# Performance work log

Hardware: AMD Instinct MI355X
Metric: run time of the kernel (lower is better)

The kernel has to match this reference:

```python
import jax, jax.numpy as jnp
import numpy as np

SPATIAL = 128   # N: wall spatial resolution
CROP = 256      # M: temporal bins (power of 2)
BIN_LEN = 0.01
WALL_SIZE = 2.0


def _grids():
    # Reproduces parpareparam(): normalized freq-domain coordinate grids, [2M,2N,2N].
    M, N = CROP, SPATIAL
    width = WALL_SIZE / 2.0
    trange = CROP * BIN_LEN  # crop * c * (bin_len / c)
    zdim = (np.arange(2 * M, dtype=np.float32) - M) / M
    xdim = (np.arange(2 * N, dtype=np.float32) - N) / N
    gz = np.ascontiguousarray(np.broadcast_to(zdim[:, None, None], (2 * M, 2 * N, 2 * N)))
    gy = np.ascontiguousarray(np.broadcast_to(xdim[None, :, None], (2 * M, 2 * N, 2 * N)))
    gx = np.ascontiguousarray(np.broadcast_to(xdim[None, None, :], (2 * M, 2 * N, 2 * N)))
    fkrange = (N * trange / (M * width * 4.0)) ** 2
    gznew = np.sqrt(fkrange * (gx ** 2 + gy ** 2) + gz ** 2).astype(np.float32)
    return jnp.asarray(gx), jnp.asarray(gy), jnp.asarray(gz), jnp.asarray(gznew)


def _grid_sample_3d(vol, x, y, z):
    """Trilinear grid sample, padding_mode='zeros', align_corners=False.
    vol: [B, D, H, W] (complex ok); x/y/z: [Dg,Hg,Wg] in [-1,1] (x->W, y->H, z->D)."""
    B, D, H, W = vol.shape
    ix = ((x + 1.0) * W - 1.0) * 0.5
    iy = ((y + 1.0) * H - 1.0) * 0.5
    iz = ((z + 1.0) * D - 1.0) * 0.5
    ix0 = jnp.floor(ix); iy0 = jnp.floor(iy); iz0 = jnp.floor(iz)
    fx = ix - ix0; fy = iy - iy0; fz = iz - iz0
    ix0 = ix0.astype(jnp.int32); iy0 = iy0.astype(jnp.int32); iz0 = iz0.astype(jnp.int32)
    out = jnp.zeros((B,) + x.shape, vol.dtype)
    for dz in (0, 1):
        for dy in (0, 1):
            for dx in (0, 1):
                xi = ix0 + dx; yi = iy0 + dy; zi = iz0 + dz
                valid = (xi >= 0) & (xi < W) & (yi >= 0) & (yi < H) & (zi >= 0) & (zi < D)
                w = ((fx if dx else 1.0 - fx) * (fy if dy else 1.0 - fy) * (fz if dz else 1.0 - fz))
                w = jnp.where(valid, w, 0.0)
                xi = jnp.clip(xi, 0, W - 1); yi = jnp.clip(yi, 0, H - 1); zi = jnp.clip(zi, 0, D - 1)
                out = out + vol[:, zi, yi, xi] * w  # gather 8 trilinear corners
    return out


def _fk_forward(feat_padded):
    # feat_padded: [B, Dn, CROP, N, N] float32
    B, Dn, T, H, W = feat_padded.shape
    M, N = CROP, SPATIAL
    gx, gy, gz, gznew = _grids()
    gridz = jnp.arange(M, dtype=jnp.float32) / (M - 1)  # gridz_1xMx1x1
    data = feat_padded.reshape(B * Dn, M, N, N) * (gridz ** 2)[None, :, None, None]
    data = jax.nn.relu(data)
    # sqrt with grad-safe double-where (torch sqrt backward at 0 is nan; math limit here is 0)
    data = jnp.where(data > 0, jnp.sqrt(jnp.where(data > 0, data, 1.0)), 0.0)
    pad = jnp.zeros((B * Dn, 2 * M, 2 * N, 2 * N), jnp.float32).at[:, :M, :N, :N].set(data)
    fre = jnp.fft.fftn(pad, axes=(1, 2, 3))            # torch.rfft(x,3,onesided=False)
    fre = jnp.roll(fre, (M, N, N), axis=(1, 2, 3))      # fftshift rolls
    t = _grid_sample_3d(fre, gx, gy, gznew)             # Stolt frequency resampling
    t = t.at[:, :M + 1].set(0.0)                        # z0pos = M+1 (first zdim>0)
    t = t * (jnp.abs(gz) / (gznew + 1e-8))[None]        # |f_z| Jacobian scaling
    t = jnp.roll(t, (M, N, N), axis=(1, 2, 3))          # ifftshift (even dims)
    vol = jnp.fft.ifftn(t, axes=(1, 2, 3))[:, :M, :N, :N]
    out = vol.real ** 2 + vol.imag ** 2                 # squared magnitude
    return out.reshape(B, Dn, M, N, N)


def setup_inputs() -> dict:
    key = jax.random.key(0)
    feat = jax.random.uniform(key, (1, 1, CROP, SPATIAL, SPATIAL), dtype=jnp.float32)
    return {"feture_bxdxtxhxw": feat, "tbes": 0, "tens": CROP}


def reference(feture_bxdxtxhxw, tbes, tens):
    tbe, ten = int(tbes), int(tens)
    featpad = jnp.pad(feture_bxdxtxhxw, ((0, 0), (0, 0), (tbe, CROP - ten), (0, 0), (0, 0)))
    return _fk_forward(featpad)
```

## Files before the change

### kernel.cpp

```cpp
#include <hip/hip_runtime.h>


typedef float __attribute__((ext_vector_type(2))) cpx;

__device__ float4 g_tw4[512];

__device__ __forceinline__ cpx cswap(cpx a){ return __builtin_shufflevector(a, a, 1, 0); }
__device__ __forceinline__ cpx cmji(cpx a){ return cswap(a)*(cpx){1.0f, -1.0f}; }
__device__ __forceinline__ cpx cmpi(cpx a){ return cswap(a)*(cpx){-1.0f, 1.0f}; }

__device__ __forceinline__ int rev4_8(int k){
    return ((k & 3) << 6) | ((k & 12) << 2) | ((k >> 2) & 12) | (k >> 6);
}
__device__ __forceinline__ int rev8_9(int k){
    return ((k & 7) << 6) | (k & 56) | (k >> 6);
}

__global__ void k_tw(){
    int j = threadIdx.x;
    double a = -2.0*3.14159265358979323846*(double)j/512.0;
    float c = (float)cos(a), s = (float)sin(a);
    g_tw4[j] = make_float4(c, c, -s, s);
}

template<bool INV>
__device__ __forceinline__ cpx twmul(cpx a, int k){
    float4 t = g_tw4[k & 511];
    cpx wl = {t.x, t.y};
    cpx wh = {t.z, t.w};
    cpx r = a*wl;
    return INV ? (r - cswap(a)*wh) : (r + cswap(a)*wh);
}

template<bool INV>
__device__ __forceinline__ void dft4(cpx* x){
    cpx e0 = x[0] + x[2], e1 = x[0] - x[2];
    cpx o0 = x[1] + x[3], o1 = x[1] - x[3];
    x[0] = e0 + o0;
    x[2] = e0 - o0;
    cpx j1 = INV ? cmpi(o1) : cmji(o1);
    x[1] = e1 + j1;
    x[3] = e1 - j1;
}

template<bool INV>
__device__ __forceinline__ void dft4_h2(cpx* x){
    cpx a0 = x[0], a1 = x[1];
    x[0] = a0 + a1;
    x[2] = a0 - a1;
    cpx j1 = INV ? cmpi(a1) : cmji(a1);
    x[1] = a0 + j1;
    x[3] = a0 - j1;
}

template<bool INV>
__device__ __forceinline__ void dft4_lo2(cpx* x){
    cpx e0 = x[0] + x[2], e1 = x[0] - x[2];
    cpx o0 = x[1] + x[3], o1 = x[1] - x[3];
    x[0] = e0 + o0;
    x[1] = e1 + (INV ? cmpi(o1) : cmji(o1));
}

template<bool INV>
__device__ __forceinline__ void dft8(cpx* x){
    const float s = 0.70710678118654752440f;
    cpx e0 = x[0] + x[4], e2 = x[0] - x[4];
    cpx e1 = x[2] + x[6], e3 = x[2] - x[6];
    cpx E0 = e0 + e1, E2 = e0 - e1;
    cpx j3 = INV ? cmpi(e3) : cmji(e3);
    cpx E1 = e2 + j3, E3 = e2 - j3;
    cpx o0 = x[1] + x[5], o2 = x[1] - x[5];
    cpx o1 = x[3] + x[7], o3 = x[3] - x[7];
    cpx O0 = o0 + o1, O2 = o0 - o1;
    cpx k3 = INV ? cmpi(o3) : cmji(o3);
    cpx O1 = o2 + k3, O3 = o2 - k3;
    cpx W1, W2, W3;
    if (!INV){
        W1 = s*(O1 + cmji(O1));
        W2 = cmji(O2);
        W3 = s*(cmji(O3) - O3);
    } else {
        W1 = s*(O1 + cmpi(O1));
        W2 = cmpi(O2);
        W3 = s*(cmpi(O3) - O3);
    }
    x[0] = E0 + O0; x[4] = E0 - O0;
    x[1] = E1 + W1; x[5] = E1 - W1;
    x[2] = E2 + W2; x[6] = E2 - W2;
    x[3] = E3 + W3; x[7] = E3 - W3;
}

template<bool INV>
__device__ __forceinline__ void dft8_h4(cpx* x){
    const float s = 0.70710678118654752440f;
    cpx a0 = x[0], a1 = x[1], a2 = x[2], a3 = x[3];
    cpx E0 = a0 + a2, E2 = a0 - a2;
    cpx j3 = INV ? cmpi(a2) : cmji(a2);
    cpx E1 = a0 + j3, E3 = a0 - j3;
    cpx O0 = a1 + a3, O2 = a1 - a3;
    cpx k3 = INV ? cmpi(a3) : cmji(a3);
    cpx O1 = a1 + k3, O3 = a1 - k3;
    cpx W1, W2, W3;
    if (!INV){
        W1 = s*(O1 + cmji(O1));
        W2 = cmji(O2);
        W3 = s*(cmji(O3) - O3);
    } else {
        W1 = s*(O1 + cmpi(O1));
        W2 = cmpi(O2);
        W3 = s*(cmpi(O3) - O3);
    }
    x[0] = E0 + O0; x[4] = E0 - O0;
    x[1] = E1 + W1; x[5] = E1 - W1;
    x[2] = E2 + W2; x[6] = E2 - W2;
    x[3] = E3 + W3; x[7] = E3 - W3;
}

template<bool INV>
__device__ __forceinline__ void dft8_lo4(cpx* x){
    const float s = 0.70710678118654752440f;
    cpx e0 = x[0] + x[4], e2 = x[0] - x[4];
    cpx e1 = x[2] + x[6], e3 = x[2] - x[6];
    cpx E0 = e0 + e1, E2 = e0 - e1;
    cpx j3 = INV ? cmpi(e3) : cmji(e3);
    cpx E1 = e2 + j3, E3 = e2 - j3;
    cpx o0 = x[1] + x[5], o2 = x[1] - x[5];
    cpx o1 = x[3] + x[7], o3 = x[3] - x[7];
    cpx O0 = o0 + o1, O2 = o0 - o1;
    cpx k3 = INV ? cmpi(o3) : cmji(o3);
    cpx O1 = o2 + k3, O3 = o2 - k3;
    cpx W1, W2, W3;
    if (!INV){
        W1 = s*(O1 + cmji(O1));
        W2 = cmji(O2);
        W3 = s*(cmji(O3) - O3);
    } else {
        W1 = s*(O1 + cmpi(O1));
        W2 = cmpi(O2);
        W3 = s*(cmpi(O3) - O3);
    }
    x[0] = E0 + O0;
    x[1] = E1 + W1;
    x[2] = E2 + W2;
    x[3] = E3 + W3;
}

template<bool INV, bool CROP>
__device__ __forceinline__ void fft256_r4_tail(cpx* sl, int b){
    cpx x[4];
    {
        int j = b & 15, g = (b >> 4) << 6;
        #pragma unroll
        for (int t = 0; t < 4; ++t) x[t] = sl[g + j + (t << 4)];
        dft4<INV>(x);
        #pragma unroll
        for (int r = 1; r < 4; ++r) x[r] = twmul<INV>(x[r], 8*j*r);
        #pragma unroll
        for (int r = 0; r < 4; ++r) sl[g + j + (r << 4)] = x[r];
    }
    __syncthreads();
    {
        int j = b & 3, g = (b >> 2) << 4;
        #pragma unroll
        for (int t = 0; t < 4; ++t) x[t] = sl[g + j + (t << 2)];
        dft4<INV>(x);
        #pragma unroll
        for (int r = 1; r < 4; ++r) x[r] = twmul<INV>(x[r], 32*j*r);
        #pragma unroll
        for (int r = 0; r < 4; ++r) sl[g + j + (r << 2)] = x[r];
    }
    __syncthreads();
    {
        int g = b << 2;
        #pragma unroll
        for (int t = 0; t < 4; ++t) x[t] = sl[g + t];
        if (CROP){
            dft4_lo2<INV>(x);
            sl[g] = x[0]; sl[g + 1] = x[1];
        } else {
            dft4<INV>(x);
            #pragma unroll
            for (int r = 0; r < 4; ++r) sl[g + r] = x[r];
        }
    }
    __syncthreads();
}

__global__ __launch_bounds__(256) void k_fft_x_fill(const float* __restrict__ feat, cpx* __restrict__ V){
    __shared__ cpx s[4*256];
    int tid = threadIdx.x;
    int line0 = blockIdx.x << 2;
    int l = tid >> 6, b = tid & 63;
    int line = line0 + l;
    cpx* sl = s + l*256;
    {
        int z = line >> 7;
        float g = (float)z*(1.0f/255.0f);
        const float* fl = feat + ((size_t)line << 7);
        float a  = fl[b]*g*g;       a  = a  > 0.0f ? sqrtf(a)  : 0.0f;
        float bb = fl[b + 64]*g*g;  bb = bb > 0.0f ? sqrtf(bb) : 0.0f;
        cpx x[4];
        x[0] = (cpx){a, 0.0f};
        x[1] = (cpx){bb, 0.0f};
        dft4_h2<false>(x);
        #pragma unroll
        for (int r = 1; r < 4; ++r) x[r] = twmul<false>(x[r], 2*b*r);
        #pragma unroll
        for (int r = 0; r < 4; ++r) sl[b + (r << 6)] = x[r];
    }
    __syncthreads();
    fft256_r4_tail<false, false>(sl, b);
    for (int i = tid; i < 4*128; i += 256){
        int ll = i >> 7, f4 = i & 127;
        int lin = line0 + ll;
        int base = ((lin >> 7) << 16) + ((lin & 127) << 8);
        const cpx* sll = s + ll*256;
        int e0 = 2*f4;
        cpx Fm = e0 ? sll[rev4_8(e0 - 1) ^ 2] : (cpx){0.0f, 0.0f};
        cpx F0 = sll[rev4_8(e0) ^ 2];
        cpx F1 = sll[rev4_8(e0 + 1) ^ 2];
        cpx o0 = 0.5f*(Fm + F0);
        cpx o1 = 0.5f*(F0 + F1);
        float4 o = make_float4(o0.x, o0.y, o1.x, o1.y);
        ((float4*)(V + base))[f4] = o;
    }
}

__global__ __launch_bounds__(256) void k_fft_x_inv_mag(const cpx* __restrict__ W,
                                                       float* __restrict__ out){
    __shared__ cpx s[4*256];
    int tid = threadIdx.x;
    int line0 = blockIdx.x << 2;
    int l = tid >> 6, b = tid & 63;
    int line = line0 + l;
    int base = ((line >> 7) << 16) + ((line & 127) << 8);
    cpx* sl = s + l*256;
    {
        cpx x[4];
        #pragma unroll
        for (int t = 0; t < 4; ++t) x[t] = W[base + b + (t << 6)];
        dft4<true>(x);
        #pragma unroll
        for (int r = 1; r < 4; ++r) x[r] = twmul<true>(x[r], 2*b*r);
        #pragma unroll
        for (int r = 0; r < 4; ++r) sl[b + (r << 6)] = x[r];
    }
    __syncthreads();
    fft256_r4_tail<true, true>(sl, b);
    {
        int z = line >> 7, y = line & 127;
        cpx v0 = sl[rev4_8(2*b)];
        cpx v1 = sl[rev4_8(2*b + 1)];
        const float SC2 = (1.0f/33554432.0f)*(1.0f/33554432.0f);
        float2 o = make_float2((v0.x*v0.x + v0.y*v0.y)*SC2,
                               (v1.x*v1.x + v1.y*v1.y)*SC2);
        ((float2*)(out + (((size_t)(z*128 + y)) << 7)))[b] = o;
    }
}

template<bool INV, bool HALF_IN, bool HALF_OUT>
__global__ __launch_bounds__(1024) void k_fft_y(cpx* __restrict__ V){
    __shared__ cpx s[256*16];
    int tid = threadIdx.x;
    int z  = blockIdx.x >> 4;
    int x0 = (blockIdx.x & 15) << 4;
    int base = (z << 16) + x0;
    int c = tid & 15, idx = tid >> 4;
    cpx x[4];
    {
        int j = idx;
        if (HALF_IN){
            x[0] = V[base + (j << 8) + c];
            x[1] = V[base + ((j + 64) << 8) + c];
            dft4_h2<INV>(x);
        } else {
            #pragma unroll
            for (int t = 0; t < 4; ++t) x[t] = V[base + ((j + (t << 6)) << 8) + c];
            dft4<INV>(x);
        }
        #pragma unroll
        for (int r = 1; r < 4; ++r) x[r] = twmul<INV>(x[r], 2*j*r);
        #pragma unroll
        for (int r = 0; r < 4; ++r) s[(j + (r << 6))*16 + c] = x[r];
    }
    __syncthreads();
    {
        int j = idx & 15, g = (idx >> 4) << 6;
        #pragma unroll
        for (int t = 0; t < 4; ++t) x[t] = s[(g + j + (t << 4))*16 + c];
        dft4<INV>(x);
        #pragma unroll
        for (int r = 1; r < 4; ++r) x[r] = twmul<INV>(x[r], 8*j*r);
        #pragma unroll
        for (int r = 0; r < 4; ++r) s[(g + j + (r << 4))*16 + c] = x[r];
    }
    __syncthreads();
    {
        int j = idx & 3, g = (idx >> 2) << 4;
        #pragma unroll
        for (int t = 0; t < 4; ++t) x[t] = s[(g + j + (t << 2))*16 + c];
        dft4<INV>(x);
        #pragma unroll
        for (int r = 1; r < 4; ++r) x[r] = twmul<INV>(x[r], 32*j*r);
        #pragma unroll
        for (int r = 0; r < 4; ++r) s[(g + j + (r << 2))*16 + c] = x[r];
    }
    __syncthreads();
    if (HALF_OUT){
        int g = idx << 2;
        #pragma unroll
        for (int t = 0; t < 4; ++t) x[t] = s[(g + t)*16 + c];
        dft4_lo2<INV>(x);
        int e0 = rev4_8(g);
        V[base + (e0 << 8) + c] = x[0];
        V[base + ((e0 + 64) << 8) + c] = x[1];
        return;
    }
    {
        int g = idx << 2;
        #pragma unroll
        for (int t = 0; t < 4; ++t) x[t] = s[(g + t)*16 + c];
        dft4<INV>(x);
        #pragma unroll
        for (int r = 0; r < 4; ++r) s[(g + r)*16 + c] = x[r];
    }
    __syncthreads();
    for (int i = tid; i < 256*8; i += 1024){
        int f4c = i & 7, e = i >> 3;
        int p0 = rev4_8(e) ^ 2;
        float4 S0 = ((const float4*)(s + p0*16))[f4c];
        float4 S1 = make_float4(0.0f, 0.0f, 0.0f, 0.0f);
        if (e){
            int p1 = rev4_8(e - 1) ^ 2;
            S1 = ((const float4*)(s + p1*16))[f4c];
        }
        float4 o;
        o.x = 0.5f*(S0.x + S1.x); o.y = 0.5f*(S0.y + S1.y);
        o.z = 0.5f*(S0.z + S1.z); o.w = 0.5f*(S0.w + S1.w);
        ((float4*)(V + base + (e << 8)))[f4c] = o;
    }
}

__global__ __launch_bounds__(1024, 8) void k_fftz_fused(cpx* __restrict__ V){
    __shared__ cpx s[512*16];
    int tid = threadIdx.x;
    int yD  = blockIdx.x >> 4;
    int x0D = (blockIdx.x & 15) << 4;
    int baseD = (yD << 8) + x0D;
    int yS  = (yD + 128) & 255;
    int x0S = (x0D + 128) & 255;
    int baseS = (yS << 8) + x0S;
    int c = tid & 15, idx = tid >> 4;
    cpx x[8];
    int j = idx;
    {
        #pragma unroll
        for (int t = 0; t < 4; ++t)
            x[t] = V[baseS + (((size_t)(j + (t << 6))) << 16) + c];
        dft8_h4<false>(x);
        #pragma unroll
        for (int r = 1; r < 8; ++r) x[r] = twmul<false>(x[r], j*r);
        #pragma unroll
        for (int r = 0; r < 8; ++r) s[(j + (r << 6))*16 + c] = x[r];
    }
    __syncthreads();
    {
        int jj = idx & 7, g = (idx >> 3) << 6;
        #pragma unroll
        for (int t = 0; t < 8; ++t) x[t] = s[(g + jj + (t << 3))*16 + c];
        dft8<false>(x);
        #pragma unroll
        for (int r = 1; r < 8; ++r) x[r] = twmul<false>(x[r], 8*jj*r);
        #pragma unroll
        for (int r = 0; r < 8; ++r) s[(g + jj + (r << 3))*16 + c] = x[r];
    }
    __syncthreads();
    {
        int g = idx << 3;
        #pragma unroll
        for (int t = 0; t < 8; ++t) x[t] = s[(g + t)*16 + c];
        dft8_lo4<false>(x);
        #pragma unroll
        for (int r = 0; r < 4; ++r){
            int e = (r << 6) | ((idx & 7) << 3) | (idx >> 3);
            s[e*16 + c] = x[r];
        }
    }
    __syncthreads();
    {
        int xs = x0S + c;
        float gx = (float)(xs - 128)*(1.0f/128.0f);
        float gy = (float)(yS - 128)*(1.0f/128.0f);
        float rxy = 0.1024f*(gx*gx + gy*gy);
        #pragma unroll
        for (int t = 0; t < 4; ++t){
            int zd = j + (t << 6);
            cpx r = (cpx){0.0f, 0.0f};
            if (zd){
                float gz = (float)zd*(1.0f/256.0f);
                float gzn = sqrtf(rxy + gz*gz);
                float iz = ((gzn + 1.0f)*512.0f - 1.0f)*0.5f;
                float fiz = floorf(iz);
                int iz0 = (int)fiz;
                float fz = iz - fiz;
                float sc = gz/(gzn + 1e-8f);
                int b0 = (iz0 < 511 ? iz0 : 511) - 256;
                int b1 = ((iz0 + 1) < 511 ? (iz0 + 1) : 511) - 256;
                float w0 = (iz0     <= 511) ? (1.0f - fz)*sc : 0.0f;
                float w1 = (iz0 + 1 <= 511) ? fz*sc : 0.0f;
                cpx a = s[(b0 << 4) + c];
                cpx b = s[(b1 << 4) + c];
                r = a*w0 + b*w1;
            }
            x[t] = r;
        }
        dft8_h4<true>(x);
        #pragma unroll
        for (int r = 1; r < 8; ++r) x[r] = twmul<true>(x[r], j*r);
    }
    __syncthreads();
    {
        #pragma unroll
        for (int r = 0; r < 8; ++r) s[(j + (r << 6))*16 + c] = x[r];
    }
    __syncthreads();
    {
        int jj = idx & 7, g = (idx >> 3) << 6;
        #pragma unroll
        for (int t = 0; t < 8; ++t) x[t] = s[(g + jj + (t << 3))*16 + c];
        dft8<true>(x);
        #pragma unroll
        for (int r = 1; r < 8; ++r) x[r] = twmul<true>(x[r], 8*jj*r);
        #pragma unroll
        for (int r = 0; r < 8; ++r) s[(g + jj + (r << 3))*16 + c] = x[r];
    }
    __syncthreads();
    {
        int g = idx << 3;
        #pragma unroll
        for (int t = 0; t < 8; ++t) x[t] = s[(g + t)*16 + c];
        dft8_lo4<true>(x);
        #pragma unroll
        for (int r = 0; r < 4; ++r){
            int e = (r << 6) | ((idx & 7) << 3) | (idx >> 3);
            V[baseD + (((size_t)(e + 256)) << 16) + c] = x[r];
        }
    }
}

extern "C" void kernel_launch(void* const* d_in, const int* in_sizes, int n_in,
                              void* d_out, int out_size, void* d_ws, size_t ws_size,
                              hipStream_t stream){
    const float* feat = (const float*)d_in[0];
    float* out = (float*)d_out;

    const size_t WS_NEED = (size_t)512*256*256*8;
    if (ws_size < WS_NEED){
        hipMemsetAsync(d_out, 0, (size_t)out_size*sizeof(float), stream);
        return;
    }
    cpx* V  = (cpx*)d_ws;
    cpx* Vu = V + (size_t)256*65536;

    k_tw<<<1, 512, 0, stream>>>();
    k_fft_x_fill<<<8192, 256, 0, stream>>>(feat, V);
    k_fft_y<false, true, false><<<4096, 1024, 0, stream>>>(V);
    k_fftz_fused<<<4096, 1024, 0, stream>>>(V);
    k_fft_y<true, false, true><<<4096, 1024, 0, stream>>>(Vu);
    k_fft_x_inv_mag<<<8192, 256, 0, stream>>>(Vu, out);
}
```

Before: 258.6 us.

## Restructure Y-axis FFT as two radix-16 passes with 256-thread blocks

The 256-point Y-axis FFT goes from four radix-4 passes with 1024 threads per block to two in-register radix-16 passes (16x16 decomposition) with 256 threads per block. This removes two shared-memory round trips and barriers and pads the shared row stride to 18 to reduce bank conflicts. In exchange each thread holds 16 complex values, which raises register pressure and may lower occupancy. The launch configuration changes to match.

Measured after the change: 250.8 us. 3.0% less time.

```diff
diff --git a/kernel.cpp b/kernel.cpp
--- a/kernel.cpp
+++ b/kernel.cpp
@@ -2,6 +2,7 @@
 
 
 typedef float __attribute__((ext_vector_type(2))) cpx;
+typedef float __attribute__((ext_vector_type(4))) cpx2;
 
 __device__ float4 g_tw4[512];
 
@@ -12,9 +13,7 @@
 __device__ __forceinline__ int rev4_8(int k){
     return ((k & 3) << 6) | ((k & 12) << 2) | ((k >> 2) & 12) | (k >> 6);
 }
-__device__ __forceinline__ int rev8_9(int k){
-    return ((k & 7) << 6) | (k & 56) | (k >> 6);
-}
+__device__ __forceinline__ int prm(int q){ return ((q & 3) << 2) | (q >> 2); }
 
 __global__ void k_tw(){
     int j = threadIdx.x;
@@ -42,7 +41,6 @@
     x[1] = e1 + j1;
     x[3] = e1 - j1;
 }
-
 template<bool INV>
 __device__ __forceinline__ void dft4_h2(cpx* x){
     cpx a0 = x[0], a1 = x[1];
@@ -52,13 +50,59 @@
     x[1] = a0 + j1;
     x[3] = a0 - j1;
 }
-
 template<bool INV>
 __device__ __forceinline__ void dft4_lo2(cpx* x){
     cpx e0 = x[0] + x[2], e1 = x[0] - x[2];
     cpx o0 = x[1] + x[3], o1 = x[1] - x[3];
     x[0] = e0 + o0;
     x[1] = e1 + (INV ? cmpi(o1) : cmji(o1));
+}
+
+template<bool INV>
+__device__ __forceinline__ void dft16(cpx* x){
+    #pragma unroll
+    for (int j2 = 0; j2 < 4; ++j2){
+        cpx y[4] = {x[j2], x[j2+4], x[j2+8], x[j2+12]};
+        dft4<INV>(y);
+        if (j2){
+            #pragma unroll
+            for (int r = 1; r < 4; ++r) y[r] = twmul<INV>(y[r], 32*j2*r);
+        }
+        x[j2] = y[0]; x[j2+4] = y[1]; x[j2+8] = y[2]; x[j2+12] = y[3];
+    }
+    #pragma unroll
+    for (int g = 0; g < 16; g += 4) dft4<INV>(x + g);
+}
+template<bool INV>
+__device__ __forceinline__ void dft16_h8(cpx* x){
+    #pragma unroll
+    for (int j2 = 0; j2 < 4; ++j2){
+        cpx y[4];
+        y[0] = x[j2]; y[1] = x[j2+4];
+        dft4_h2<INV>(y);
+        if (j2){
+            #pragma unroll
+            for (int r = 1; r < 4; ++r) y[r] = twmul<INV>(y[r], 32*j2*r);
+        }
+        x[j2] = y[0]; x[j2+4] = y[1]; x[j2+8] = y[2]; x[j2+12] = y[3];
+    }
+    #pragma unroll
+    for (int g = 0; g < 16; g += 4) dft4<INV>(x + g);
+}
+template<bool INV>
+__device__ __forceinline__ void dft16_lo8(cpx* x){
+    #pragma unroll
+    for (int j2 = 0; j2 < 4; ++j2){
+        cpx y[4] = {x[j2], x[j2+4], x[j2+8], x[j2+12]};
+        dft4<INV>(y);
+        if (j2){
+            #pragma unroll
+            for (int r = 1; r < 4; ++r) y[r] = twmul<INV>(y[r], 32*j2*r);
+        }
+        x[j2] = y[0]; x[j2+4] = y[1]; x[j2+8] = y[2]; x[j2+12] = y[3];
+    }
+    #pragma unroll
+    for (int g = 0; g < 16; g += 4) dft4_lo2<INV>(x + g);
 }
 
 template<bool INV>
@@ -89,7 +133,6 @@
     x[2] = E2 + W2; x[6] = E2 - W2;
     x[3] = E3 + W3; x[7] = E3 - W3;
 }
-
 template<bool INV>
 __device__ __forceinline__ void dft8_h4(cpx* x){
     const float s = 0.70710678118654752440f;
@@ -115,7 +158,6 @@
     x[2] = E2 + W2; x[6] = E2 - W2;
     x[3] = E3 + W3; x[7] = E3 - W3;
 }
-
 template<bool INV>
 __device__ __forceinline__ void dft8_lo4(cpx* x){
     const float s = 0.70710678118654752440f;
@@ -258,86 +300,63 @@
     }
 }
 
+#define YROW 18
 template<bool INV, bool HALF_IN, bool HALF_OUT>
-__global__ __launch_bounds__(1024) void k_fft_y(cpx* __restrict__ V){
-    __shared__ cpx s[256*16];
+__global__ __launch_bounds__(256, 4) void k_fft_y(cpx* __restrict__ V){
+    __shared__ cpx s[256*YROW];
     int tid = threadIdx.x;
     int z  = blockIdx.x >> 4;
     int x0 = (blockIdx.x & 15) << 4;
     int base = (z << 16) + x0;
-    int c = tid & 15, idx = tid >> 4;
-    cpx x[4];
-    {
-        int j = idx;
+    int c = tid & 15, j = tid >> 4;
+    cpx x[16];
+    {
         if (HALF_IN){
-            x[0] = V[base + (j << 8) + c];
-            x[1] = V[base + ((j + 64) << 8) + c];
-            dft4_h2<INV>(x);
+            #pragma unroll
+            for (int t = 0; t < 8; ++t) x[t] = V[base + ((j + (t << 4)) << 8) + c];
+            dft16_h8<INV>(x);
         } else {
             #pragma unroll
-            for (int t = 0; t < 4; ++t) x[t] = V[base + ((j + (t << 6)) << 8) + c];
-            dft4<INV>(x);
-        }
-        #pragma unroll
-        for (int r = 1; r < 4; ++r) x[r] = twmul<INV>(x[r], 2*j*r);
-        #pragma unroll
-        for (int r = 0; r < 4; ++r) s[(j + (r << 6))*16 + c] = x[r];
-    }
-    __syncthreads();
-    {
-        int j = idx & 15, g = (idx >> 4) << 6;
-        #pragma unroll
-        for (int t = 0; t < 4; ++t) x[t] = s[(g + j + (t << 4))*16 + c];
-        dft4<INV>(x);
-        #pragma unroll
-        for (int r = 1; r < 4; ++r) x[r] = twmul<INV>(x[r], 8*j*r);
-        #pragma unroll
-        for (int r = 0; r < 4; ++r) s[(g + j + (r << 4))*16 + c] = x[r];
-    }
-    __syncthreads();
-    {
-        int j = idx & 3, g = (idx >> 2) << 4;
-        #pragma unroll
-        for (int t = 0; t < 4; ++t) x[t] = s[(g + j + (t << 2))*16 + c];
-        dft4<INV>(x);
-        #pragma unroll
-        for (int r = 1; r < 4; ++r) x[r] = twmul<INV>(x[r], 32*j*r);
-        #pragma unroll
-        for (int r = 0; r < 4; ++r) s[(g + j + (r << 2))*16 + c] = x[r];
-    }
-    __syncthreads();
+            for (int t = 0; t < 16; ++t) x[t] = V[base + ((j + (t << 4)) << 8) + c];
+            dft16<INV>(x);
+        }
+        #pragma unroll
+        for (int r = 1; r < 16; ++r) x[prm(r)] = twmul<INV>(x[prm(r)], 2*j*r);
+        #pragma unroll
+        for (int r = 0; r < 16; ++r) s[(j + (r << 4))*YROW + c] = x[prm(r)];
+    }
+    __syncthreads();
+    int g = j << 4;
     if (HALF_OUT){
-        int g = idx << 2;
-        #pragma unroll
-        for (int t = 0; t < 4; ++t) x[t] = s[(g + t)*16 + c];
-        dft4_lo2<INV>(x);
-        int e0 = rev4_8(g);
-        V[base + (e0 << 8) + c] = x[0];
-        V[base + ((e0 + 64) << 8) + c] = x[1];
+        #pragma unroll
+        for (int t = 0; t < 16; ++t) x[t] = s[(g + t)*YROW + c];
+        dft16_lo8<INV>(x);
+        #pragma unroll
+        for (int sb = 0; sb < 8; ++sb)
+            V[base + (((sb << 4) | j) << 8) + c] = x[prm(sb)];
         return;
     }
     {
-        int g = idx << 2;
-        #pragma unroll
-        for (int t = 0; t < 4; ++t) x[t] = s[(g + t)*16 + c];
-        dft4<INV>(x);
-        #pragma unroll
-        for (int r = 0; r < 4; ++r) s[(g + r)*16 + c] = x[r];
-    }
-    __syncthreads();
-    for (int i = tid; i < 256*8; i += 1024){
+        #pragma unroll
+        for (int t = 0; t < 16; ++t) x[t] = s[(g + t)*YROW + c];
+        dft16<INV>(x);
+        #pragma unroll
+        for (int u = 0; u < 16; ++u) s[(g + u)*YROW + c] = x[u];
+    }
+    __syncthreads();
+    for (int i = tid; i < 256*8; i += 256){
         int f4c = i & 7, e = i >> 3;
-        int p0 = rev4_8(e) ^ 2;
-        float4 S0 = ((const float4*)(s + p0*16))[f4c];
-        float4 S1 = make_float4(0.0f, 0.0f, 0.0f, 0.0f);
+        int k0 = e ^ 128;
+        int r0 = ((k0 & 15) << 4) | prm(k0 >> 4);
+        cpx2 S0 = ((const cpx2*)(s + r0*YROW))[f4c];
+        cpx2 S1 = (cpx2){0.0f, 0.0f, 0.0f, 0.0f};
         if (e){
-            int p1 = rev4_8(e - 1) ^ 2;
-            S1 = ((const float4*)(s + p1*16))[f4c];
-        }
-        float4 o;
-        o.x = 0.5f*(S0.x + S1.x); o.y = 0.5f*(S0.y + S1.y);
-        o.z = 0.5f*(S0.z + S1.z); o.w = 0.5f*(S0.w + S1.w);
-        ((float4*)(V + base + (e << 8)))[f4c] = o;
+            int k1 = (e - 1) ^ 128;
+            int r1 = ((k1 & 15) << 4) | prm(k1 >> 4);
+            S1 = ((const cpx2*)(s + r1*YROW))[f4c];
+        }
+        cpx2 o = 0.5f*(S0 + S1);
+        ((cpx2*)(V + base + (e << 8)))[f4c] = o;
     }
 }
 
@@ -464,8 +483,8 @@
 
     k_tw<<<1, 512, 0, stream>>>();
     k_fft_x_fill<<<8192, 256, 0, stream>>>(feat, V);
-    k_fft_y<false, true, false><<<4096, 1024, 0, stream>>>(V);
+    k_fft_y<false, true, false><<<4096, 256, 0, stream>>>(V);
     k_fftz_fused<<<4096, 1024, 0, stream>>>(V);
-    k_fft_y<true, false, true><<<4096, 1024, 0, stream>>>(Vu);
+    k_fft_y<true, false, true><<<4096, 256, 0, stream>>>(Vu);
     k_fft_x_inv_mag<<<8192, 256, 0, stream>>>(Vu, out);
 }
```
